# Kernel optimization log

Hardware: AMD Instinct MI355X
Metric: run time of the kernel (lower is better)

## Reference

```python
import jax, jax.numpy as jnp
import numpy as np

INPUT_DIM = 1024
OUTPUT_DIM = 1024


def setup_inputs() -> dict:
    key = jax.random.key(0)
    k1, k2, k3, k4 = jax.random.split(key, 4)
    B, S, D = 4, 2048, INPUT_DIM
    src = jax.random.normal(k1, (B, S, D), dtype=jnp.float32)
    tgt = jax.random.normal(k2, (B, S, D), dtype=jnp.float32)
    # nn.Linear(input_dim*2, output_dim): weight [out, in], bias [out]
    bound = 1.0 / np.sqrt(2 * D)
    W = jax.random.uniform(k3, (OUTPUT_DIM, 2 * D), jnp.float32, -bound, bound)
    b = jax.random.uniform(k4, (OUTPUT_DIM,), jnp.float32, -bound, bound)
    return {"src": src, "tgt": tgt, "W": W, "b": b}


def reference(src, tgt, W, b):
    # weight = bmm(tgt, src^T): [B, S_tgt, S_src]
    weight = jnp.einsum("btd,bsd->bts", tgt, src)
    # NOTE: original uses Softmax(dim=1) -> normalizes over the tgt axis
    weight = jax.nn.softmax(weight, axis=1)
    # weighted sum over src positions: [B, S_tgt, D]
    weight_sum = jnp.einsum("bts,bsd->btd", weight, src)
    output = jnp.concatenate([weight_sum, tgt], axis=2)  # [B, S_tgt, 2D]
    output = output @ W.T + b  # [B, S_tgt, output_dim]
    return (output, weight)
```

## Files before the change

### kernel.cpp

```cpp
#include <hip/hip_runtime.h>
#include <stdint.h>


#define B_   4
#define S_   2048
#define D_   1024
#define OUTD 1024

typedef unsigned short ushort_t;
typedef _Float16 half8 __attribute__((ext_vector_type(8)));
typedef float    f32x4 __attribute__((ext_vector_type(4)));

__device__ __forceinline__ ushort_t f2h(float f) {
    union { _Float16 h; ushort_t u; } v;
    v.h = (_Float16)f;
    return v.u;
}
__device__ __forceinline__ float h2f(ushort_t u) {
    union { _Float16 h; ushort_t u; } v;
    v.u = u;
    return (float)v.h;
}

__device__ __forceinline__ void ld16(const ushort_t* g, ushort_t* l) {
    __builtin_amdgcn_global_load_lds(
        (const __attribute__((address_space(1))) void*)g,
        (__attribute__((address_space(3))) void*)l, 16, 0, 0);
}


__global__ void k_split(const float4* __restrict__ src, const float4* __restrict__ tgt,
                        ushort4* __restrict__ sh,
                        ushort4* __restrict__ th, ushort4* __restrict__ tl)
{
    const int64_t n4 = (int64_t)B_ * S_ * D_ / 4;
    for (int64_t i = (int64_t)blockIdx.x * blockDim.x + threadIdx.x; i < n4;
         i += (int64_t)gridDim.x * blockDim.x) {
        float4 s = src[i];
        sh[i] = (ushort4){f2h(s.x), f2h(s.y), f2h(s.z), f2h(s.w)};
        float4 tv = tgt[i];
        ushort4 ht = {f2h(tv.x), f2h(tv.y), f2h(tv.z), f2h(tv.w)};
        th[i] = ht;
        tl[i] = (ushort4){f2h(tv.x - h2f(ht.x)), f2h(tv.y - h2f(ht.y)),
                          f2h(tv.z - h2f(ht.z)), f2h(tv.w - h2f(ht.w))};
    }
}

__global__ void k_wconv(const float4* __restrict__ W, ushort4* __restrict__ wb)
{
    const int64_t n4 = (int64_t)OUTD * 2 * D_ / 4;
    for (int64_t i = (int64_t)blockIdx.x * blockDim.x + threadIdx.x; i < n4;
         i += (int64_t)gridDim.x * blockDim.x) {
        float4 w = W[i];
        wb[i] = (ushort4){f2h(w.x), f2h(w.y), f2h(w.z), f2h(w.w)};
    }
}

__launch_bounds__(512, 2)
__global__ void k_gemm_logits(const ushort_t* __restrict__ Ah, const ushort_t* __restrict__ Al,
                              const ushort_t* __restrict__ Bs,
                              float* __restrict__ C,
                              float* __restrict__ pm, float* __restrict__ ps)
{
    const int M = S_, N = S_, K = D_;
    int b = blockIdx.z;
    Ah += (int64_t)b * M * K;  Al += (int64_t)b * M * K;
    Bs += (int64_t)b * N * K;
    C  += (int64_t)b * M * N;

    __shared__ __align__(16) ushort_t lds[3 * 24576];
    __shared__ float red_m[2][256], red_s[2][256];

    int t    = threadIdx.x;
    int m0   = blockIdx.y * 256, n0 = blockIdx.x * 256;
    int wave = t >> 6, lane = t & 63;
    int wr   = (wave >> 2) * 128;
    int wc   = (wave & 3) * 64;
    int l15  = lane & 15, quad = lane >> 4;

    f32x4 acc[8][4];
#pragma unroll
    for (int i = 0; i < 8; i++)
#pragma unroll
        for (int j = 0; j < 4; j++) acc[i][j] = (f32x4){0.f, 0.f, 0.f, 0.f};

    int pr   = t >> 3;
    int slot = t & 7;
    int cg   = slot ^ (pr & 7);
    int srow = pr * 2 + (cg >> 2);
    int scol = (cg & 3) * 8;

    const ushort_t* gAh = Ah + (int64_t)(m0 + srow) * K + scol;
    const ushort_t* gAl = Al + (int64_t)(m0 + srow) * K + scol;
    const ushort_t* gB  = Bs + (int64_t)(n0 + srow) * K + scol;
    const int64_t rstep = (int64_t)128 * K;

    auto stage_all = [&](int bufi, int kofs) {
        ushort_t* Lb = lds + bufi * 24576 + t * 8;
        ld16(gAh + kofs,         Lb);
        ld16(gAh + rstep + kofs, Lb + 4096);
        ld16(gAl + kofs,         Lb + 8192);
        ld16(gAl + rstep + kofs, Lb + 12288);
        ld16(gB  + kofs,         Lb + 16384);
        ld16(gB  + rstep + kofs, Lb + 20480);
    };

    int aoff[8], boff[4];
#pragma unroll
    for (int i = 0; i < 8; i++) {
        int R = wr + i * 16 + l15;
        int p = R >> 1, c = ((R & 1) << 2) + quad;
        aoff[i] = p * 64 + ((c ^ (p & 7)) << 3);
    }
#pragma unroll
    for (int j = 0; j < 4; j++) {
        int R = wc + j * 16 + l15;
        int p = R >> 1, c = ((R & 1) << 2) + quad;
        boff[j] = p * 64 + ((c ^ (p & 7)) << 3);
    }

    const int NT = 32;
    stage_all(0, 0);
    stage_all(1, 32);

    for (int kt = 0; kt < NT; ++kt) {
        const ushort_t* Lb = lds + (kt % 3) * 24576;
        ushort_t* Ld = lds + ((kt + 2) % 3) * 24576 + t * 8;
        const int nofs = (kt + 2) * 32;
        const bool pre = (kt + 2) < NT;

        if (kt + 1 < NT) {
            asm volatile("s_waitcnt vmcnt(6)" ::: "memory");
        } else {
            asm volatile("s_waitcnt vmcnt(0)" ::: "memory");
        }
        __builtin_amdgcn_s_barrier();
        asm volatile("" ::: "memory");
        __builtin_amdgcn_sched_barrier(0);

        half8 av[4], bf[4];

#pragma unroll
        for (int j = 0; j < 4; j++) bf[j] = *(const half8*)(Lb + 16384 + boff[j]);
#pragma unroll
        for (int i = 0; i < 4; i++) av[i] = *(const half8*)(Lb + aoff[i]);
        if (pre) { ld16(gAh + nofs, Ld);  ld16(gAh + rstep + nofs, Ld + 4096); }
        __builtin_amdgcn_s_barrier();
        __builtin_amdgcn_s_setprio(1);
#pragma unroll
        for (int i = 0; i < 4; i++)
#pragma unroll
            for (int j = 0; j < 4; j++)
                acc[i][j] = __builtin_amdgcn_mfma_f32_16x16x32_f16(av[i], bf[j], acc[i][j], 0, 0, 0);
        __builtin_amdgcn_s_setprio(0);
        __builtin_amdgcn_s_barrier();

#pragma unroll
        for (int i = 0; i < 4; i++) av[i] = *(const half8*)(Lb + 8192 + aoff[i]);
        if (pre) { ld16(gAl + nofs, Ld + 8192);  ld16(gAl + rstep + nofs, Ld + 12288); }
        __builtin_amdgcn_s_barrier();
        __builtin_amdgcn_s_setprio(1);
#pragma unroll
        for (int i = 0; i < 4; i++)
#pragma unroll
            for (int j = 0; j < 4; j++)
                acc[i][j] = __builtin_amdgcn_mfma_f32_16x16x32_f16(av[i], bf[j], acc[i][j], 0, 0, 0);
        __builtin_amdgcn_s_setprio(0);
        __builtin_amdgcn_s_barrier();

#pragma unroll
        for (int i = 0; i < 4; i++) av[i] = *(const half8*)(Lb + aoff[4 + i]);
        if (pre) { ld16(gB + nofs, Ld + 16384);  ld16(gB + rstep + nofs, Ld + 20480); }
        __builtin_amdgcn_s_barrier();
        __builtin_amdgcn_s_setprio(1);
#pragma unroll
        for (int i = 0; i < 4; i++)
#pragma unroll
            for (int j = 0; j < 4; j++)
                acc[4 + i][j] = __builtin_amdgcn_mfma_f32_16x16x32_f16(av[i], bf[j], acc[4 + i][j], 0, 0, 0);
        __builtin_amdgcn_s_setprio(0);
        __builtin_amdgcn_s_barrier();

#pragma unroll
        for (int i = 0; i < 4; i++) av[i] = *(const half8*)(Lb + 8192 + aoff[4 + i]);
        __builtin_amdgcn_s_barrier();
        __builtin_amdgcn_s_setprio(1);
#pragma unroll
        for (int i = 0; i < 4; i++)
#pragma unroll
            for (int j = 0; j < 4; j++)
                acc[4 + i][j] = __builtin_amdgcn_mfma_f32_16x16x32_f16(av[i], bf[j], acc[4 + i][j], 0, 0, 0);
        __builtin_amdgcn_s_setprio(0);
    }

#pragma unroll
    for (int i = 0; i < 8; i++) {
        int row_base = m0 + wr + i * 16 + quad * 4;
#pragma unroll
        for (int j = 0; j < 4; j++) {
            int col = n0 + wc + j * 16 + l15;
#pragma unroll
            for (int r = 0; r < 4; r++)
                C[(int64_t)(row_base + r) * N + col] = acc[i][j][r];
        }
    }

    int wrow = wave >> 2;
#pragma unroll
    for (int j = 0; j < 4; j++) {
        float m = -3.0e38f;
#pragma unroll
        for (int i = 0; i < 8; i++)
#pragma unroll
            for (int r = 0; r < 4; r++) m = fmaxf(m, acc[i][j][r]);
        float s = 0.f;
#pragma unroll
        for (int i = 0; i < 8; i++)
#pragma unroll
            for (int r = 0; r < 4; r++) s += __expf(acc[i][j][r] - m);
#pragma unroll
        for (int d = 16; d <= 32; d <<= 1) {
            float m2 = __shfl_xor(m, d, 64);
            float s2 = __shfl_xor(s, d, 64);
            float nm = fmaxf(m, m2);
            s = s * __expf(m - nm) + s2 * __expf(m2 - nm);
            m = nm;
        }
        if (lane < 16) {
            red_m[wrow][wc + j * 16 + l15] = m;
            red_s[wrow][wc + j * 16 + l15] = s;
        }
    }
    __syncthreads();
    if (t < 256) {
        float ma = red_m[0][t], mb = red_m[1][t];
        float sa = red_s[0][t], sb = red_s[1][t];
        float m = fmaxf(ma, mb);
        float s = sa * __expf(ma - m) + sb * __expf(mb - m);
        int idx = blockIdx.y * (B_ * S_) + b * S_ + n0 + t;
        pm[idx] = m;
        ps[idx] = s;
    }
}


__global__ void k_colstats2(const float* __restrict__ pm, const float* __restrict__ ps,
                            float* __restrict__ cmax, float* __restrict__ cinv)
{
    int i = blockIdx.x * 256 + threadIdx.x;
    float m = -3.0e38f;
#pragma unroll
    for (int c = 0; c < 8; c++) m = fmaxf(m, pm[c * (B_ * S_) + i]);
    float sum = 0.f;
#pragma unroll
    for (int c = 0; c < 8; c++) sum += ps[c * (B_ * S_) + i] * __expf(pm[c * (B_ * S_) + i] - m);
    cmax[i] = m;
    cinv[i] = 1.0f / sum;
}

__global__ void k_softmax_norm(float4* __restrict__ L, const float4* __restrict__ cmax4,
                               const float4* __restrict__ cinv4, ushort4* __restrict__ wbf)
{
    const int64_t n4 = (int64_t)B_ * S_ * S_ / 4;
    for (int64_t i = (int64_t)blockIdx.x * blockDim.x + threadIdx.x; i < n4;
         i += (int64_t)gridDim.x * blockDim.x) {
        int b  = (int)(i >> 20);
        int c4 = (int)(i & 511);
        float4 x  = L[i];
        float4 cm = cmax4[b * 512 + c4];
        float4 ci = cinv4[b * 512 + c4];
        float4 w;
        w.x = __expf(x.x - cm.x) * ci.x;
        w.y = __expf(x.y - cm.y) * ci.y;
        w.z = __expf(x.z - cm.z) * ci.z;
        w.w = __expf(x.w - cm.w) * ci.w;
        L[i] = w;
        wbf[i] = (ushort4){f2h(w.x), f2h(w.y), f2h(w.z), f2h(w.w)};
    }
}

__launch_bounds__(512, 2)
__global__ void k_gemm_nt2(const ushort_t* __restrict__ A, int lda, int64_t bsA,
                           const ushort_t* __restrict__ Bm, int ldb, int64_t bsB,
                           ushort_t* __restrict__ C, int ldc, int64_t bsC, int K)
{
    int b = blockIdx.z;
    A  += (int64_t)b * bsA;
    Bm += (int64_t)b * bsB;
    C  += (int64_t)b * bsC;

    __shared__ __align__(16) ushort_t lds[3 * 24576];

    int t    = threadIdx.x;
    int m0   = blockIdx.y * 256, n0 = blockIdx.x * 128;
    int wave = t >> 6, lane = t & 63;
    int wr   = (wave >> 1) * 64;
    int wc   = (wave & 1) * 64;
    int l15  = lane & 15, quad = lane >> 4;

    f32x4 acc[4][4];
#pragma unroll
    for (int i = 0; i < 4; i++)
#pragma unroll
        for (int j = 0; j < 4; j++) acc[i][j] = (f32x4){0.f, 0.f, 0.f, 0.f};

    int srow = t >> 3;
    int cg   = (t & 7) ^ (srow & 7);
    int scol = cg * 8;

    const ushort_t* gA = A  + (int64_t)(m0 + srow) * lda + scol;
    const ushort_t* gB = Bm + (int64_t)(n0 + srow) * ldb + scol;

    auto stage = [&](int bufi, int k0) {
        ushort_t* Lb = lds + bufi * 24576 + t * 8;
        ld16(gA + k0,                        Lb);
        ld16(gA + (int64_t)64  * lda + k0,   Lb + 4096);
        ld16(gA + (int64_t)128 * lda + k0,   Lb + 8192);
        ld16(gA + (int64_t)192 * lda + k0,   Lb + 12288);
        ld16(gB + k0,                        Lb + 16384);
        ld16(gB + (int64_t)64  * ldb + k0,   Lb + 20480);
    };

    int aoff[4][2], boff[4][2];
#pragma unroll
    for (int i = 0; i < 4; i++) {
        int R = wr + i * 16 + l15;
#pragma unroll
        for (int h = 0; h < 2; h++) {
            int c = quad + h * 4;
            aoff[i][h] = R * 64 + ((c ^ (R & 7)) << 3);
        }
    }
#pragma unroll
    for (int j = 0; j < 4; j++) {
        int R = wc + j * 16 + l15;
#pragma unroll
        for (int h = 0; h < 2; h++) {
            int c = quad + h * 4;
            boff[j][h] = 16384 + R * 64 + ((c ^ (R & 7)) << 3);
        }
    }

    const int NT = K >> 6;
    stage(0, 0);
    stage(1, 64);

    for (int kt = 0; kt < NT; ++kt) {
        if (kt + 1 < NT) {
            asm volatile("s_waitcnt vmcnt(6)" ::: "memory");
        } else {
            asm volatile("s_waitcnt vmcnt(0)" ::: "memory");
        }
        __builtin_amdgcn_s_barrier();
        asm volatile("" ::: "memory");
        __builtin_amdgcn_sched_barrier(0);

        if (kt + 2 < NT) stage((kt + 2) % 3, (kt + 2) * 64);

        const ushort_t* Lb = lds + (kt % 3) * 24576;
#pragma unroll
        for (int h = 0; h < 2; h++) {
            half8 af[4], bf[4];
#pragma unroll
            for (int i = 0; i < 4; i++) af[i] = *(const half8*)(Lb + aoff[i][h]);
#pragma unroll
            for (int j = 0; j < 4; j++) bf[j] = *(const half8*)(Lb + boff[j][h]);
            __builtin_amdgcn_s_setprio(1);
#pragma unroll
            for (int i = 0; i < 4; i++)
#pragma unroll
                for (int j = 0; j < 4; j++)
                    acc[i][j] = __builtin_amdgcn_mfma_f32_16x16x32_f16(af[i], bf[j], acc[i][j], 0, 0, 0);
            __builtin_amdgcn_s_setprio(0);
        }
    }

#pragma unroll
    for (int i = 0; i < 4; i++) {
        int row_base = m0 + wr + i * 16 + quad * 4;
#pragma unroll
        for (int j = 0; j < 4; j++) {
            int col = n0 + wc + j * 16 + l15;
#pragma unroll
            for (int r = 0; r < 4; r++)
                C[(int64_t)(row_base + r) * ldc + col] = f2h(acc[i][j][r]);
        }
    }
}

__launch_bounds__(512, 2)
__global__ void k_gemm_final(const ushort_t* __restrict__ Wt, const ushort_t* __restrict__ PT,
                             const ushort_t* __restrict__ Q, const float* __restrict__ bias,
                             float* __restrict__ out)
{
    const int K = S_, N = OUTD;
    int b = blockIdx.z;
    const ushort_t* A  = Wt + (int64_t)b * S_ * S_;
    const ushort_t* Bm = PT + (int64_t)b * OUTD * S_;
    const ushort_t* Qb = Q  + (int64_t)b * S_ * OUTD;
    float* Cb = out + (int64_t)b * S_ * OUTD;

    __shared__ __align__(16) ushort_t lds[3 * 24576];

    int t    = threadIdx.x;
    int m0   = blockIdx.y * 256, n0 = blockIdx.x * 128;
    int wave = t >> 6, lane = t & 63;
    int wr   = (wave >> 1) * 64;
    int wc   = (wave & 1) * 64;
    int l15  = lane & 15, quad = lane >> 4;

    f32x4 acc[4][4];
#pragma unroll
    for (int i = 0; i < 4; i++)
#pragma unroll
        for (int j = 0; j < 4; j++) acc[i][j] = (f32x4){0.f, 0.f, 0.f, 0.f};

    int srow = t >> 3;
    int cg   = (t & 7) ^ (srow & 7);
    int scol = cg * 8;

    const ushort_t* gA = A  + (int64_t)(m0 + srow) * K + scol;
    const ushort_t* gB = Bm + (int64_t)(n0 + srow) * K + scol;

    auto stage = [&](int bufi, int k0) {
        ushort_t* Lb = lds + bufi * 24576 + t * 8;
        ld16(gA + k0,                      Lb);
        ld16(gA + (int64_t)64  * K + k0,   Lb + 4096);
        ld16(gA + (int64_t)128 * K + k0,   Lb + 8192);
        ld16(gA + (int64_t)192 * K + k0,   Lb + 12288);
        ld16(gB + k0,                      Lb + 16384);
        ld16(gB + (int64_t)64  * K + k0,   Lb + 20480);
    };

    int aoff[4][2], boff[4][2];
#pragma unroll
    for (int i = 0; i < 4; i++) {
        int R = wr + i * 16 + l15;
#pragma unroll
        for (int h = 0; h < 2; h++) {
            int c = quad + h * 4;
            aoff[i][h] = R * 64 + ((c ^ (R & 7)) << 3);
        }
    }
#pragma unroll
    for (int j = 0; j < 4; j++) {
        int R = wc + j * 16 + l15;
#pragma unroll
        for (int h = 0; h < 2; h++) {
            int c = quad + h * 4;
            boff[j][h] = 16384 + R * 64 + ((c ^ (R & 7)) << 3);
        }
    }

    const int NT = K >> 6;
    stage(0, 0);
    stage(1, 64);

    for (int kt = 0; kt < NT; ++kt) {
        if (kt + 1 < NT) {
            asm volatile("s_waitcnt vmcnt(6)" ::: "memory");
        } else {
            asm volatile("s_waitcnt vmcnt(0)" ::: "memory");
        }
        __builtin_amdgcn_s_barrier();
        asm volatile("" ::: "memory");
        __builtin_amdgcn_sched_barrier(0);

        if (kt + 2 < NT) stage((kt + 2) % 3, (kt + 2) * 64);

        const ushort_t* Lb = lds + (kt % 3) * 24576;
#pragma unroll
        for (int h = 0; h < 2; h++) {
            half8 af[4], bf[4];
#pragma unroll
            for (int i = 0; i < 4; i++) af[i] = *(const half8*)(Lb + aoff[i][h]);
#pragma unroll
            for (int j = 0; j < 4; j++) bf[j] = *(const half8*)(Lb + boff[j][h]);
            __builtin_amdgcn_s_setprio(1);
#pragma unroll
            for (int i = 0; i < 4; i++)
#pragma unroll
                for (int j = 0; j < 4; j++)
                    acc[i][j] = __builtin_amdgcn_mfma_f32_16x16x32_f16(af[i], bf[j], acc[i][j], 0, 0, 0);
            __builtin_amdgcn_s_setprio(0);
        }
    }

#pragma unroll
    for (int i = 0; i < 4; i++) {
        int row_base = m0 + wr + i * 16 + quad * 4;
#pragma unroll
        for (int j = 0; j < 4; j++) {
            int col = n0 + wc + j * 16 + l15;
            float bv = bias[col];
#pragma unroll
            for (int r = 0; r < 4; r++) {
                int64_t idx = (int64_t)(row_base + r) * N + col;
                Cb[idx] = acc[i][j][r] + h2f(Qb[idx]) + bv;
            }
        }
    }
}


extern "C" void kernel_launch(void* const* d_in, const int* in_sizes, int n_in,
                              void* d_out, int out_size, void* d_ws, size_t ws_size,
                              hipStream_t stream)
{
    const float* src  = (const float*)d_in[0];
    const float* tgt  = (const float*)d_in[1];
    const float* W    = (const float*)d_in[2];
    const float* bias = (const float*)d_in[3];

    float* out = (float*)d_out;
    float* Lw  = out + (size_t)B_ * S_ * OUTD;

    char*  ws = (char*)d_ws;
    size_t o  = 0;
    auto take = [&](size_t bytes) -> char* {
        char* p = ws + o;
        o += (bytes + 255) & ~(size_t)255;
        return p;
    };
    const size_t ELEMS = (size_t)B_ * S_ * D_;
    ushort_t* sh   = (ushort_t*)take(ELEMS * 2);
    ushort_t* th   = (ushort_t*)take(ELEMS * 2);
    ushort_t* tl   = (ushort_t*)take(ELEMS * 2);
    ushort_t* wbf  = (ushort_t*)take((size_t)B_ * S_ * S_ * 2);
    ushort_t* wb   = (ushort_t*)take((size_t)OUTD * 2 * D_ * 2);
    ushort_t* PT   = (ushort_t*)take((size_t)B_ * OUTD * S_ * 2);
    ushort_t* Qb   = (ushort_t*)take((size_t)B_ * S_ * OUTD * 2);
    float*    pm   = (float*)take(16 * (size_t)B_ * S_ * 4);
    float*    ps   = (float*)take(16 * (size_t)B_ * S_ * 4);
    float*    cmax = (float*)take((size_t)B_ * S_ * 4);
    float*    cinv = (float*)take((size_t)B_ * S_ * 4);
    (void)ws_size; (void)in_sizes; (void)n_in; (void)out_size;

    k_split<<<dim3(2048), dim3(256), 0, stream>>>((const float4*)src, (const float4*)tgt,
                                                  (ushort4*)sh, (ushort4*)th, (ushort4*)tl);
    k_wconv<<<dim3(512), dim3(256), 0, stream>>>((const float4*)W, (ushort4*)wb);

    k_gemm_nt2<<<dim3(16, 4, 4), dim3(512), 0, stream>>>(
        wb, 2 * D_, 0,
        sh, D_, (int64_t)S_ * D_,
        PT, S_, (int64_t)OUTD * S_, D_);

    k_gemm_nt2<<<dim3(8, 8, 4), dim3(512), 0, stream>>>(
        th, D_, (int64_t)S_ * D_,
        wb + D_, 2 * D_, 0,
        Qb, OUTD, (int64_t)S_ * OUTD, D_);

    k_gemm_logits<<<dim3(8, 8, 4), dim3(512), 0, stream>>>(th, tl, sh, Lw, pm, ps);

    k_colstats2<<<dim3(32), dim3(256), 0, stream>>>(pm, ps, cmax, cinv);
    k_softmax_norm<<<dim3(2048), dim3(256), 0, stream>>>((float4*)Lw, (const float4*)cmax,
                                                         (const float4*)cinv, (ushort4*)wbf);

    k_gemm_final<<<dim3(8, 8, 4), dim3(512), 0, stream>>>(wbf, PT, Qb, bias, out);
}
```

Baseline: 347.7 us.

## Merge conversion kernels and projection GEMMs, interleave prefetch with MFMA halves

Folds the W fp16 conversion into the src/tgt split kernel and merges the two independent projection GEMMs into a single launch with a flat block index that dispatches to either problem. The GEMM main loops (nt2 and final) now split the next-tile global-to-LDS prefetch into two halves issued between the two MFMA k-halves, with extra barriers. The goals are to cut launch overhead, fill the GPU with 512 blocks at once, and spread load issue across compute. The extra barriers per iteration add synchronization cost.

```diff
diff --git a/kernel.cpp b/kernel.cpp
--- a/kernel.cpp
+++ b/kernel.cpp
@@ -30,29 +30,28 @@
 
 
 __global__ void k_split(const float4* __restrict__ src, const float4* __restrict__ tgt,
+                        const float4* __restrict__ W,
                         ushort4* __restrict__ sh,
-                        ushort4* __restrict__ th, ushort4* __restrict__ tl)
+                        ushort4* __restrict__ th, ushort4* __restrict__ tl,
+                        ushort4* __restrict__ wb)
 {
     const int64_t n4 = (int64_t)B_ * S_ * D_ / 4;
-    for (int64_t i = (int64_t)blockIdx.x * blockDim.x + threadIdx.x; i < n4;
+    const int64_t w4 = (int64_t)OUTD * 2 * D_ / 4;
+    for (int64_t i = (int64_t)blockIdx.x * blockDim.x + threadIdx.x; i < n4 + w4;
          i += (int64_t)gridDim.x * blockDim.x) {
-        float4 s = src[i];
-        sh[i] = (ushort4){f2h(s.x), f2h(s.y), f2h(s.z), f2h(s.w)};
-        float4 tv = tgt[i];
-        ushort4 ht = {f2h(tv.x), f2h(tv.y), f2h(tv.z), f2h(tv.w)};
-        th[i] = ht;
-        tl[i] = (ushort4){f2h(tv.x - h2f(ht.x)), f2h(tv.y - h2f(ht.y)),
-                          f2h(tv.z - h2f(ht.z)), f2h(tv.w - h2f(ht.w))};
-    }
-}
-
-__global__ void k_wconv(const float4* __restrict__ W, ushort4* __restrict__ wb)
-{
-    const int64_t n4 = (int64_t)OUTD * 2 * D_ / 4;
-    for (int64_t i = (int64_t)blockIdx.x * blockDim.x + threadIdx.x; i < n4;
-         i += (int64_t)gridDim.x * blockDim.x) {
-        float4 w = W[i];
-        wb[i] = (ushort4){f2h(w.x), f2h(w.y), f2h(w.z), f2h(w.w)};
+        if (i < n4) {
+            float4 s = src[i];
+            sh[i] = (ushort4){f2h(s.x), f2h(s.y), f2h(s.z), f2h(s.w)};
+            float4 tv = tgt[i];
+            ushort4 ht = {f2h(tv.x), f2h(tv.y), f2h(tv.z), f2h(tv.w)};
+            th[i] = ht;
+            tl[i] = (ushort4){f2h(tv.x - h2f(ht.x)), f2h(tv.y - h2f(ht.y)),
+                              f2h(tv.z - h2f(ht.z)), f2h(tv.w - h2f(ht.w))};
+        } else {
+            int64_t j = i - n4;
+            float4 w = W[j];
+            wb[j] = (ushort4){f2h(w.x), f2h(w.y), f2h(w.z), f2h(w.w)};
+        }
     }
 }
 
@@ -280,19 +279,35 @@
 }
 
 __launch_bounds__(512, 2)
-__global__ void k_gemm_nt2(const ushort_t* __restrict__ A, int lda, int64_t bsA,
-                           const ushort_t* __restrict__ Bm, int ldb, int64_t bsB,
-                           ushort_t* __restrict__ C, int ldc, int64_t bsC, int K)
+__global__ void k_gemm_nt2(const ushort_t* __restrict__ A0, int lda0, int64_t bsA0,
+                           const ushort_t* __restrict__ B0, int ldb0, int64_t bsB0,
+                           ushort_t* __restrict__ C0, int ldc0, int64_t bsC0,
+                           const ushort_t* __restrict__ A1, int lda1, int64_t bsA1,
+                           const ushort_t* __restrict__ B1, int ldb1, int64_t bsB1,
+                           ushort_t* __restrict__ C1, int ldc1, int64_t bsC1)
 {
-    int b = blockIdx.z;
-    A  += (int64_t)b * bsA;
-    Bm += (int64_t)b * bsB;
-    C  += (int64_t)b * bsC;
+    const int K = D_;
+    int id = blockIdx.x;
+    const ushort_t *A, *Bm;
+    ushort_t* C;
+    int lda, ldb, ldc, bx, by;
+    if (id < 256) {
+        int b = id >> 6;
+        by = (id >> 4) & 3;  bx = id & 15;
+        A = A0 + (int64_t)b * bsA0;  Bm = B0 + (int64_t)b * bsB0;  C = C0 + (int64_t)b * bsC0;
+        lda = lda0; ldb = ldb0; ldc = ldc0;
+    } else {
+        int i2 = id - 256;
+        int b = i2 >> 6;
+        by = (i2 >> 3) & 7;  bx = i2 & 7;
+        A = A1 + (int64_t)b * bsA1;  Bm = B1 + (int64_t)b * bsB1;  C = C1 + (int64_t)b * bsC1;
+        lda = lda1; ldb = ldb1; ldc = ldc1;
+    }
 
     __shared__ __align__(16) ushort_t lds[3 * 24576];
 
     int t    = threadIdx.x;
-    int m0   = blockIdx.y * 256, n0 = blockIdx.x * 128;
+    int m0   = by * 256, n0 = bx * 128;
     int wave = t >> 6, lane = t & 63;
     int wr   = (wave >> 1) * 64;
     int wc   = (wave & 1) * 64;
@@ -346,6 +361,11 @@
     stage(1, 64);
 
     for (int kt = 0; kt < NT; ++kt) {
+        const ushort_t* Lb = lds + (kt % 3) * 24576;
+        ushort_t* Ld = lds + ((kt + 2) % 3) * 24576 + t * 8;
+        const int nofs = (kt + 2) * 64;
+        const bool pre = (kt + 2) < NT;
+
         if (kt + 1 < NT) {
             asm volatile("s_waitcnt vmcnt(6)" ::: "memory");
         } else {
@@ -355,24 +375,44 @@
         asm volatile("" ::: "memory");
         __builtin_amdgcn_sched_barrier(0);
 
-        if (kt + 2 < NT) stage((kt + 2) % 3, (kt + 2) * 64);
-
-        const ushort_t* Lb = lds + (kt % 3) * 24576;
-#pragma unroll
-        for (int h = 0; h < 2; h++) {
-            half8 af[4], bf[4];
-#pragma unroll
-            for (int i = 0; i < 4; i++) af[i] = *(const half8*)(Lb + aoff[i][h]);
-#pragma unroll
-            for (int j = 0; j < 4; j++) bf[j] = *(const half8*)(Lb + boff[j][h]);
-            __builtin_amdgcn_s_setprio(1);
-#pragma unroll
-            for (int i = 0; i < 4; i++)
-#pragma unroll
-                for (int j = 0; j < 4; j++)
-                    acc[i][j] = __builtin_amdgcn_mfma_f32_16x16x32_f16(af[i], bf[j], acc[i][j], 0, 0, 0);
-            __builtin_amdgcn_s_setprio(0);
-        }
+        half8 af[4], bf[4];
+
+#pragma unroll
+        for (int i = 0; i < 4; i++) af[i] = *(const half8*)(Lb + aoff[i][0]);
+#pragma unroll
+        for (int j = 0; j < 4; j++) bf[j] = *(const half8*)(Lb + boff[j][0]);
+        if (pre) {
+            ld16(gA + nofs,                      Ld);
+            ld16(gA + (int64_t)64  * lda + nofs, Ld + 4096);
+            ld16(gA + (int64_t)128 * lda + nofs, Ld + 8192);
+        }
+        __builtin_amdgcn_s_barrier();
+        __builtin_amdgcn_s_setprio(1);
+#pragma unroll
+        for (int i = 0; i < 4; i++)
+#pragma unroll
+            for (int j = 0; j < 4; j++)
+                acc[i][j] = __builtin_amdgcn_mfma_f32_16x16x32_f16(af[i], bf[j], acc[i][j], 0, 0, 0);
+        __builtin_amdgcn_s_setprio(0);
+        __builtin_amdgcn_s_barrier();
+
+#pragma unroll
+        for (int i = 0; i < 4; i++) af[i] = *(const half8*)(Lb + aoff[i][1]);
+#pragma unroll
+        for (int j = 0; j < 4; j++) bf[j] = *(const half8*)(Lb + boff[j][1]);
+        if (pre) {
+            ld16(gA + (int64_t)192 * lda + nofs, Ld + 12288);
+            ld16(gB + nofs,                      Ld + 16384);
+            ld16(gB + (int64_t)64  * ldb + nofs, Ld + 20480);
+        }
+        __builtin_amdgcn_s_barrier();
+        __builtin_amdgcn_s_setprio(1);
+#pragma unroll
+        for (int i = 0; i < 4; i++)
+#pragma unroll
+            for (int j = 0; j < 4; j++)
+                acc[i][j] = __builtin_amdgcn_mfma_f32_16x16x32_f16(af[i], bf[j], acc[i][j], 0, 0, 0);
+        __builtin_amdgcn_s_setprio(0);
     }
 
 #pragma unroll
@@ -457,6 +497,11 @@
     stage(1, 64);
 
     for (int kt = 0; kt < NT; ++kt) {
+        const ushort_t* Lb = lds + (kt % 3) * 24576;
+        ushort_t* Ld = lds + ((kt + 2) % 3) * 24576 + t * 8;
+        const int nofs = (kt + 2) * 64;
+        const bool pre = (kt + 2) < NT;
+
         if (kt + 1 < NT) {
             asm volatile("s_waitcnt vmcnt(6)" ::: "memory");
         } else {
@@ -466,24 +511,44 @@
         asm volatile("" ::: "memory");
         __builtin_amdgcn_sched_barrier(0);
 
-        if (kt + 2 < NT) stage((kt + 2) % 3, (kt + 2) * 64);
-
-        const ushort_t* Lb = lds + (kt % 3) * 24576;
-#pragma unroll
-        for (int h = 0; h < 2; h++) {
-            half8 af[4], bf[4];
-#pragma unroll
-            for (int i = 0; i < 4; i++) af[i] = *(const half8*)(Lb + aoff[i][h]);
-#pragma unroll
-            for (int j = 0; j < 4; j++) bf[j] = *(const half8*)(Lb + boff[j][h]);
-            __builtin_amdgcn_s_setprio(1);
-#pragma unroll
-            for (int i = 0; i < 4; i++)
-#pragma unroll
-                for (int j = 0; j < 4; j++)
-                    acc[i][j] = __builtin_amdgcn_mfma_f32_16x16x32_f16(af[i], bf[j], acc[i][j], 0, 0, 0);
-            __builtin_amdgcn_s_setprio(0);
-        }
+        half8 af[4], bf[4];
+
+#pragma unroll
+        for (int i = 0; i < 4; i++) af[i] = *(const half8*)(Lb + aoff[i][0]);
+#pragma unroll
+        for (int j = 0; j < 4; j++) bf[j] = *(const half8*)(Lb + boff[j][0]);
+        if (pre) {
+            ld16(gA + nofs,                    Ld);
+            ld16(gA + (int64_t)64  * K + nofs, Ld + 4096);
+            ld16(gA + (int64_t)128 * K + nofs, Ld + 8192);
+        }
+        __builtin_amdgcn_s_barrier();
+        __builtin_amdgcn_s_setprio(1);
+#pragma unroll
+        for (int i = 0; i < 4; i++)
+#pragma unroll
+            for (int j = 0; j < 4; j++)
+                acc[i][j] = __builtin_amdgcn_mfma_f32_16x16x32_f16(af[i], bf[j], acc[i][j], 0, 0, 0);
+        __builtin_amdgcn_s_setprio(0);
+        __builtin_amdgcn_s_barrier();
+
+#pragma unroll
+        for (int i = 0; i < 4; i++) af[i] = *(const half8*)(Lb + aoff[i][1]);
+#pragma unroll
+        for (int j = 0; j < 4; j++) bf[j] = *(const half8*)(Lb + boff[j][1]);
+        if (pre) {
+            ld16(gA + (int64_t)192 * K + nofs, Ld + 12288);
+            ld16(gB + nofs,                    Ld + 16384);
+            ld16(gB + (int64_t)64  * K + nofs, Ld + 20480);
+        }
+        __builtin_amdgcn_s_barrier();
+        __builtin_amdgcn_s_setprio(1);
+#pragma unroll
+        for (int i = 0; i < 4; i++)
+#pragma unroll
+            for (int j = 0; j < 4; j++)
+                acc[i][j] = __builtin_amdgcn_mfma_f32_16x16x32_f16(af[i], bf[j], acc[i][j], 0, 0, 0);
+        __builtin_amdgcn_s_setprio(0);
     }
 
 #pragma unroll
@@ -536,19 +601,13 @@
     float*    cinv = (float*)take((size_t)B_ * S_ * 4);
     (void)ws_size; (void)in_sizes; (void)n_in; (void)out_size;
 
-    k_split<<<dim3(2048), dim3(256), 0, stream>>>((const float4*)src, (const float4*)tgt,
-                                                  (ushort4*)sh, (ushort4*)th, (ushort4*)tl);
-    k_wconv<<<dim3(512), dim3(256), 0, stream>>>((const float4*)W, (ushort4*)wb);
-
-    k_gemm_nt2<<<dim3(16, 4, 4), dim3(512), 0, stream>>>(
-        wb, 2 * D_, 0,
-        sh, D_, (int64_t)S_ * D_,
-        PT, S_, (int64_t)OUTD * S_, D_);
-
-    k_gemm_nt2<<<dim3(8, 8, 4), dim3(512), 0, stream>>>(
-        th, D_, (int64_t)S_ * D_,
-        wb + D_, 2 * D_, 0,
-        Qb, OUTD, (int64_t)S_ * OUTD, D_);
+    k_split<<<dim3(2560), dim3(256), 0, stream>>>(
+        (const float4*)src, (const float4*)tgt, (const float4*)W,
+        (ushort4*)sh, (ushort4*)th, (ushort4*)tl, (ushort4*)wb);
+
+    k_gemm_nt2<<<dim3(512), dim3(512), 0, stream>>>(
+        wb, 2 * D_, 0,  sh, D_, (int64_t)S_ * D_,  PT, S_, (int64_t)OUTD * S_,
+        th, D_, (int64_t)S_ * D_,  wb + D_, 2 * D_, 0,  Qb, OUTD, (int64_t)S_ * OUTD);
 
     k_gemm_logits<<<dim3(8, 8, 4), dim3(512), 0, stream>>>(th, tl, sh, Lw, pm, ps);
 
```

Result: faster. 339.6 us (-2.3%).
